# Kernel optimization log

Measured on AMD Instinct MI355X. Metric: run time of the kernel, lower is better.

The kernel has to match this reference:

```python
import jax, jax.numpy as jnp
import numpy as np

N = 50000      # nodes
E = 800000     # edges (before self-loops)
IN = 128       # in_channels
HID = 32       # hidden_channels per head
H = 4          # in_head
OUT = 40       # out_channels
OH = 1         # out_head
NEG = 0.2      # GATConv default negative_slope
EPS = 1e-5     # BatchNorm eps
SKIP = 0.5     # skip_coefficient


def setup_inputs() -> dict:
    key = jax.random.key(0)
    ks = jax.random.split(key, 24)
    s = 0.1
    f32 = jnp.float32
    return dict(
        x=jax.random.normal(ks[0], (N, IN), dtype=f32),
        W0=jax.random.normal(ks[1], (H * HID, IN), dtype=f32) * s,
        as0=jax.random.normal(ks[2], (H, HID), dtype=f32) * s,
        ad0=jax.random.normal(ks[3], (H, HID), dtype=f32) * s,
        b0=jnp.zeros((H * HID,), f32),
        g0=jnp.ones((H * HID,), f32),
        be0=jnp.zeros((H * HID,), f32),
        W1=jax.random.normal(ks[4], (H * HID, H * HID), dtype=f32) * s,
        as1=jax.random.normal(ks[5], (H, HID), dtype=f32) * s,
        ad1=jax.random.normal(ks[6], (H, HID), dtype=f32) * s,
        b1=jnp.zeros((H * HID,), f32),
        g1=jnp.ones((H * HID,), f32),
        be1=jnp.zeros((H * HID,), f32),
        W2=jax.random.normal(ks[7], (OH * OUT, H * HID), dtype=f32) * s,
        as2=jax.random.normal(ks[8], (OH, OUT), dtype=f32) * s,
        ad2=jax.random.normal(ks[9], (OH, OUT), dtype=f32) * s,
        b2=jnp.zeros((OH * OUT,), f32),
        edge_index=jax.random.randint(ks[10], (2, E), 0, N, dtype=jnp.int64),
    )


def gat_layer(x, src, dst, W, a_s, a_d, b, heads, ch):
    # PyG GATConv (concat=True): per-head linear, edge LeakyReLU attention,
    # softmax over incoming edges per destination node, scatter-add aggregate.
    n = x.shape[0]
    h = (x @ W.T).reshape(n, heads, ch)            # [N,H,C]
    al_s = jnp.einsum('nhc,hc->nh', h, a_s)        # [N,H]
    al_d = jnp.einsum('nhc,hc->nh', h, a_d)
    e = jax.nn.leaky_relu(al_s[src] + al_d[dst], NEG)   # [Etot,H]
    m = jax.ops.segment_max(e, dst, num_segments=n)     # per-dst max (stable softmax)
    ex = jnp.exp(e - m[dst])
    denom = jax.ops.segment_sum(ex, dst, num_segments=n)
    alpha = ex / denom[dst]                              # [Etot,H]
    out = jax.ops.segment_sum(alpha[:, :, None] * h[src], dst, num_segments=n)
    return out.reshape(n, heads * ch) + b


def batchnorm(x, g, b):
    # BatchNorm1d, batch-statistics form
    mu = x.mean(0)
    var = x.var(0)
    return (x - mu) * jax.lax.rsqrt(var + EPS) * g + b


def reference(x, W0, as0, ad0, b0, g0, be0, W1, as1, ad1, b1, g1, be1,
              W2, as2, ad2, b2, edge_index):
    loops = jnp.arange(N, dtype=edge_index.dtype)   # GATConv add_self_loops=True
    src = jnp.concatenate([edge_index[0], loops])
    dst = jnp.concatenate([edge_index[1], loops])
    h = jax.nn.relu(batchnorm(gat_layer(x, src, dst, W0, as0, ad0, b0, H, HID), g0, be0))
    skip = h
    h = gat_layer(h, src, dst, W1, as1, ad1, b1, H, HID)
    h = jax.nn.relu(batchnorm(h, g1, be1) + SKIP * skip)
    return gat_layer(h, src, dst, W2, as2, ad2, b2, OH, OUT)
```

## Files before the change

kernel.cpp:

```cpp
#include <hip/hip_runtime.h>
#include <hip/hip_bf16.h>
#include <stdint.h>

#define N_NODES 50000
#define N_EDGES 800000
#define TOT_EDGES (N_EDGES + N_NODES)
#define DIM 128
#define NEG 0.2f
#define BN_EPS 1e-5f
#define SKIPC 0.5f
#define NB 196
#define BCAP 6144

typedef __attribute__((ext_vector_type(8))) short short8;
typedef __attribute__((ext_vector_type(4))) float f32x4;

__device__ inline float bf2f(__hip_bfloat16 v) { return __bfloat162float(v); }
__device__ inline float u16f(unsigned short u) { return __uint_as_float(((unsigned int)u) << 16); }
__device__ inline unsigned short f2bu(float f) {
    __hip_bfloat16 b = __float2bfloat16(f);
    return *(unsigned short*)&b;
}
__device__ inline void fma8(float* acc, float ex, uint4 u) {
    acc[0] += ex * u16f((unsigned short)(u.x & 0xFFFFu));
    acc[1] += ex * u16f((unsigned short)(u.x >> 16));
    acc[2] += ex * u16f((unsigned short)(u.y & 0xFFFFu));
    acc[3] += ex * u16f((unsigned short)(u.y >> 16));
    acc[4] += ex * u16f((unsigned short)(u.z & 0xFFFFu));
    acc[5] += ex * u16f((unsigned short)(u.z >> 16));
    acc[6] += ex * u16f((unsigned short)(u.w & 0xFFFFu));
    acc[7] += ex * u16f((unsigned short)(u.w >> 16));
}
__device__ inline unsigned int pk2(float a, float b) {
    return (unsigned int)f2bu(a) | ((unsigned int)f2bu(b) << 16);
}

__global__ void zero_out_k(unsigned short* out, int n) {
    int g = blockIdx.x * 256 + threadIdx.x;
    if (g < n) out[g] = 0;
}

__global__ __launch_bounds__(256) void binA_k(const int* __restrict__ ei,
                                              int* __restrict__ bcnt,
                                              unsigned int* __restrict__ pairs) {
    __shared__ int cnt[NB], base[NB], cur[NB];
    __shared__ int sf;
    int t = threadIdx.x;
    if (t == 0) sf = 0;
    for (int i = t; i < NB; i += 256) cnt[i] = 0;
    __syncthreads();
    if (t < 16 && ei[2 * t + 1] != 0) atomicOr(&sf, 1);
    __syncthreads();
    int f = (sf == 0);
    int b0 = blockIdx.x * 4096;
    unsigned int pk[16];
    int bk[16];
    #pragma unroll
    for (int j = 0; j < 16; ++j) {
        int g = b0 + j * 256 + t;
        bk[j] = -1;
        if (g < N_EDGES) {
            int s, d;
            if (f) { s = ei[2 * g]; d = ei[2 * (N_EDGES + g)]; }
            else   { s = ei[g];     d = ei[N_EDGES + g]; }
            if ((unsigned)d < N_NODES && (unsigned)s < N_NODES) {
                bk[j] = d >> 8;
                pk[j] = (unsigned int)s | ((unsigned int)(d & 255) << 16);
                atomicAdd(&cnt[bk[j]], 1);
            }
        }
    }
    __syncthreads();
    if (t < NB) {
        int c = cnt[t];
        base[t] = c ? atomicAdd(&bcnt[t], c) : 0;
        cur[t] = 0;
    }
    __syncthreads();
    #pragma unroll
    for (int j = 0; j < 16; ++j) {
        if (bk[j] >= 0) {
            int off = base[bk[j]] + atomicAdd(&cur[bk[j]], 1);
            if (off < BCAP) pairs[(size_t)bk[j] * BCAP + off] = pk[j];
        }
    }
}

__global__ __launch_bounds__(256) void binB_k(const int* __restrict__ bcnt,
                                              const unsigned int* __restrict__ pairs,
                                              int* __restrict__ row_ptr,
                                              int* __restrict__ ssrc) {
    __shared__ int cntL[256], scanL[256], curL[256];
    __shared__ int sred[256];
    int b = blockIdx.x, t = threadIdx.x;
    int n0 = b * 256;
    int nn = min(256, N_NODES - n0);
    int cnt_b = min(bcnt[b], BCAP);
    int contrib = 0;
    if (t < b) contrib = min(bcnt[t], BCAP) + min(256, N_NODES - t * 256);
    sred[t] = contrib;
    __syncthreads();
    #pragma unroll
    for (int off = 128; off > 0; off >>= 1) {
        if (t < off) sred[t] += sred[t + off];
        __syncthreads();
    }
    int gbase = sred[0];
    if (b == NB - 1 && t == 0) row_ptr[N_NODES] = gbase + cnt_b + nn;

    const unsigned int* P = pairs + (size_t)b * BCAP;
    cntL[t] = (t < nn) ? 1 : 0;
    __syncthreads();
    for (int i = t; i < cnt_b; i += 256)
        atomicAdd(&cntL[P[i] >> 16], 1);
    __syncthreads();
    int v = cntL[t];
    scanL[t] = v;
    __syncthreads();
    for (int off = 1; off < 256; off <<= 1) {
        int x = (t >= off) ? scanL[t - off] : 0;
        __syncthreads();
        scanL[t] += x;
        __syncthreads();
    }
    int excl = scanL[t] - v;
    if (t < nn) row_ptr[n0 + t] = gbase + excl;
    curL[t] = excl;
    __syncthreads();
    if (t < nn) {
        int pos = atomicAdd(&curL[t], 1);
        ssrc[gbase + pos] = n0 + t;
    }
    for (int i = t; i < cnt_b; i += 256) {
        unsigned int p = P[i];
        int pos = atomicAdd(&curL[p >> 16], 1);
        ssrc[gbase + pos] = (int)(p & 0xFFFFu);
    }
}

struct PrepJobs { const void* src[13]; float* dst[13]; int n[13]; };
__global__ __launch_bounds__(256) void wcvt_k(const void* __restrict__ W0,
                                              const void* __restrict__ W1,
                                              const void* __restrict__ W2,
                                              unsigned short* __restrict__ Wb0,
                                              unsigned short* __restrict__ Wb1,
                                              unsigned short* __restrict__ Wb2,
                                              PrepJobs jobs,
                                              int* __restrict__ fflag) {
    __shared__ int cs;
    int t = threadIdx.x;
    if (t == 0) cs = 0;
    __syncthreads();
    {
        unsigned int w = ((const unsigned int*)W0)[t];
        float v0 = u16f((unsigned short)(w & 0xFFFFu));
        float a = fabsf(v0);
        int sane = (a < 2.0f && (a > 1e-20f || v0 == 0.0f)) ? 1 : 0;
        atomicAdd(&cs, sane);
    }
    __syncthreads();
    int f = (cs >= 128) ? 1 : 0;
    int b = blockIdx.x;
    if (b == 0 && t == 0) fflag[0] = f;
    if (b < 148) {
        int g = b * 256 + t;
        const void* W; unsigned short* Wb; int idx;
        if (g < 16384)        { W = W0; Wb = Wb0; idx = g; }
        else if (g < 32768)   { W = W1; Wb = Wb1; idx = g - 16384; }
        else if (g < 37888)   { W = W2; Wb = Wb2; idx = g - 32768; }
        else return;
        if (f) Wb[idx] = ((const unsigned short*)W)[idx];
        else   Wb[idx] = f2bu(((const float*)W)[idx]);
    } else {
        int j = b - 148;
        int n = jobs.n[j];
        const void* s = jobs.src[j];
        float* d = jobs.dst[j];
        for (int i = t; i < n; i += 256)
            d[i] = f ? bf2f(((const __hip_bfloat16*)s)[i]) : ((const float*)s)[i];
    }
}

__global__ __launch_bounds__(256) void wext_k(unsigned short* __restrict__ Wb0,
                                              unsigned short* __restrict__ Wb1,
                                              unsigned short* __restrict__ Wb2,
                                              const float* __restrict__ pAs0, const float* __restrict__ pAd0,
                                              const float* __restrict__ pAs1, const float* __restrict__ pAd1,
                                              const float* __restrict__ pAs2, const float* __restrict__ pAd2) {
    int g = blockIdx.x * 256 + threadIdx.x;
    if (g < 2048) {
        int layer = g >> 10;
        int gi = g & 1023;
        int rowq = gi >> 7;
        int k = gi & 127;
        int hh = rowq & 3, dir = rowq >> 2;
        unsigned short* Wb = layer ? Wb1 : Wb0;
        const float* p = layer ? (dir ? pAd1 : pAs1) : (dir ? pAd0 : pAs0);
        float v = 0.f;
        #pragma unroll
        for (int c = 0; c < 32; ++c)
            v += p[hh * 32 + c] * u16f(Wb[(size_t)(hh * 32 + c) * 128 + k]);
        Wb[(size_t)(128 + dir * 4 + hh) * 128 + k] = f2bu(v);
    } else if (g < 2304) {
        int gi = g - 2048;
        int dir = gi >> 7;
        int k = gi & 127;
        const float* p = dir ? pAd2 : pAs2;
        float v = 0.f;
        #pragma unroll
        for (int c = 0; c < 40; ++c)
            v += p[c] * u16f(Wb2[(size_t)c * 128 + k]);
        Wb2[(size_t)(40 + dir) * 128 + k] = f2bu(v);
    }
}

template<int MT, int MV, int ALBASE, int NH, int AMODE>
__device__ inline void mfma_body(const void* __restrict__ X,
                                 const unsigned short* __restrict__ Xprev,
                                 const unsigned short* __restrict__ Wb,
                                 unsigned short* __restrict__ Y,
                                 float* __restrict__ als, float* __restrict__ ald, int n,
                                 const float* __restrict__ bnA, const float* __restrict__ gA,
                                 const float* __restrict__ beA,
                                 const float* __restrict__ bnB, const float* __restrict__ gB,
                                 const float* __restrict__ beB) {
    const int MROWS = ALBASE + 2 * NH;
    __shared__ float sAsc[128], sAsh[128], sBsc[128], sBsh[128];
    if (AMODE >= 2) {
        int t = threadIdx.x;
        const float invN = 1.f / (float)N_NODES;
        if (t < 128) {
            float mean = bnA[t] * invN;
            float var = fmaxf(bnA[128 + t] * invN - mean * mean, 0.f);
            float s = rsqrtf(var + BN_EPS) * gA[t];
            sAsc[t] = s;
            sAsh[t] = beA[t] - mean * s;
        } else if (AMODE == 3) {
            int c = t - 128;
            float mean = bnB[c] * invN;
            float var = fmaxf(bnB[128 + c] * invN - mean * mean, 0.f);
            float s = rsqrtf(var + BN_EPS) * gB[c];
            sBsc[c] = s;
            sBsh[c] = beB[c] - mean * s;
        }
        __syncthreads();
    }
    int wave = (blockIdx.x * blockDim.x + threadIdx.x) >> 6;
    int r0 = wave * 16;
    if (r0 >= n) return;
    int lane = threadIdx.x & 63;
    int m = lane & 15, quad = lane >> 4;
    f32x4 acc[MT];
    #pragma unroll
    for (int t = 0; t < MT; ++t) acc[t] = (f32x4){0.f, 0.f, 0.f, 0.f};
    int arow = min(r0 + m, n - 1);

    #pragma unroll
    for (int kc = 0; kc < 4; ++kc) {
        int k0 = kc * 32 + quad * 8;
        short8 a;
        if (AMODE == 0) {
            const float* xp = (const float*)X + (size_t)arow * 128 + k0;
            float4 x0 = *(const float4*)xp;
            float4 x1 = *(const float4*)(xp + 4);
            a[0] = (short)f2bu(x0.x); a[1] = (short)f2bu(x0.y);
            a[2] = (short)f2bu(x0.z); a[3] = (short)f2bu(x0.w);
            a[4] = (short)f2bu(x1.x); a[5] = (short)f2bu(x1.y);
            a[6] = (short)f2bu(x1.z); a[7] = (short)f2bu(x1.w);
        } else if (AMODE == 1) {
            a = *(const short8*)((const unsigned short*)X + (size_t)arow * 128 + k0);
        } else if (AMODE == 2) {
            short8 hv = *(const short8*)((const unsigned short*)X + (size_t)arow * 128 + k0);
            #pragma unroll
            for (int j = 0; j < 8; ++j) {
                float v = u16f((unsigned short)hv[j]) * sAsc[k0 + j] + sAsh[k0 + j];
                a[j] = (short)f2bu(fmaxf(v, 0.f));
            }
        } else {
            short8 hv = *(const short8*)((const unsigned short*)X + (size_t)arow * 128 + k0);
            short8 pv = *(const short8*)(Xprev + (size_t)arow * 128 + k0);
            #pragma unroll
            for (int j = 0; j < 8; ++j) {
                float v0 = fmaxf(u16f((unsigned short)pv[j]) * sBsc[k0 + j] + sBsh[k0 + j], 0.f);
                float v = u16f((unsigned short)hv[j]) * sAsc[k0 + j] + sAsh[k0 + j] + SKIPC * v0;
                a[j] = (short)f2bu(fmaxf(v, 0.f));
            }
        }
        #pragma unroll
        for (int t = 0; t < MT; ++t) {
            int col = t * 16 + m;
            short8 b;
            if (col < MROWS) b = *(const short8*)(Wb + (size_t)col * 128 + k0);
            else             b = (short8){0,0,0,0,0,0,0,0};
            acc[t] = __builtin_amdgcn_mfma_f32_16x16x32_bf16(a, b, acc[t], 0, 0, 0);
        }
    }

    #pragma unroll
    for (int t = 0; t < MT; ++t) {
        int col = t * 16 + m;
        #pragma unroll
        for (int r = 0; r < 4; ++r) {
            int row = r0 + quad * 4 + r;
            if (row >= n) continue;
            if (col < MV) {
                Y[(size_t)row * MV + col] = f2bu(acc[t][r]);
            } else if (col < ALBASE + NH) {
                als[row * NH + (col - ALBASE)] = acc[t][r];
            } else if (col < ALBASE + 2 * NH) {
                ald[row * NH + (col - ALBASE - NH)] = acc[t][r];
            }
        }
    }
}

__global__ __launch_bounds__(256) void mfma_x_k(const void* __restrict__ X,
                                                const unsigned short* __restrict__ Wb,
                                                unsigned short* __restrict__ Y,
                                                float* __restrict__ als, float* __restrict__ ald,
                                                int n, const int* __restrict__ fflag) {
    if (fflag[0]) mfma_body<9, 128, 128, 4, 1>(X, nullptr, Wb, Y, als, ald, n,
                                               nullptr, nullptr, nullptr, nullptr, nullptr, nullptr);
    else          mfma_body<9, 128, 128, 4, 0>(X, nullptr, Wb, Y, als, ald, n,
                                               nullptr, nullptr, nullptr, nullptr, nullptr, nullptr);
}

__global__ __launch_bounds__(256) void mfma_aff_k(const unsigned short* __restrict__ X,
                                                  const unsigned short* __restrict__ Wb,
                                                  unsigned short* __restrict__ Y,
                                                  float* __restrict__ als, float* __restrict__ ald,
                                                  int n,
                                                  const float* __restrict__ bn,
                                                  const float* __restrict__ g,
                                                  const float* __restrict__ be) {
    mfma_body<9, 128, 128, 4, 2>(X, nullptr, Wb, Y, als, ald, n,
                                 bn, g, be, nullptr, nullptr, nullptr);
}

__global__ __launch_bounds__(256) void mfma_affskip_k(const unsigned short* __restrict__ X,
                                                      const unsigned short* __restrict__ Xprev,
                                                      const unsigned short* __restrict__ Wb,
                                                      unsigned short* __restrict__ Y,
                                                      float* __restrict__ als, float* __restrict__ ald,
                                                      int n,
                                                      const float* __restrict__ bnA,
                                                      const float* __restrict__ gA,
                                                      const float* __restrict__ beA,
                                                      const float* __restrict__ bnB,
                                                      const float* __restrict__ gB,
                                                      const float* __restrict__ beB) {
    mfma_body<3, 40, 40, 1, 3>(X, Xprev, Wb, Y, als, ald, n,
                               bnA, gA, beA, bnB, gB, beB);
}

template<int H, int C, int LPG, int CPL, bool FINAL>
__global__ __launch_bounds__(256) void agg4_k(const unsigned short* __restrict__ hbuf,
                                              const float* __restrict__ als,
                                              const float* __restrict__ ald,
                                              const float* __restrict__ bias,
                                              const int* __restrict__ row_ptr,
                                              const int* __restrict__ ssrc,
                                              void* __restrict__ out,
                                              const int* __restrict__ fflag, int n) {
    const int HC = H * C;
    const int G = 64 / LPG;
    const int NV = CPL / 8;
    int gw = (blockIdx.x * blockDim.x + threadIdx.x) >> 6;
    if (gw >= n) return;
    int lane = threadIdx.x & 63;
    int grp = lane / LPG;
    int sl  = lane % LPG;
    int c0 = sl * CPL;
    bool act = c0 < HC;
    int hl = act ? (c0 / C) : 0;
    int d = gw;
    int beg = row_ptr[d], end = row_ptr[d + 1];
    float adh = ald[d * H + hl];

    float denom = 0.f;
    float acc[CPL];
    #pragma unroll
    for (int j = 0; j < CPL; ++j) acc[j] = 0.f;

    int i0 = beg + grp;
    bool h0 = i0 < end;
    bool h1 = (i0 + G) < end;
    float al0 = 0.f, al1 = 0.f;
    uint4 u0[NV], u1[NV];
    if (h0) {
        int s = ssrc[i0];
        al0 = als[s * H + hl];
        if (act) {
            const uint4* hp = (const uint4*)(hbuf + (size_t)s * HC + c0);
            #pragma unroll
            for (int v = 0; v < NV; ++v) u0[v] = hp[v];
        }
    }
    if (h1) {
        int s = ssrc[i0 + G];
        al1 = als[s * H + hl];
        if (act) {
            const uint4* hp = (const uint4*)(hbuf + (size_t)s * HC + c0);
            #pragma unroll
            for (int v = 0; v < NV; ++v) u1[v] = hp[v];
        }
    }
    int inext = i0 + 2 * G;

    while (h0) {
        bool h2 = inext < end;
        float al2 = 0.f;
        uint4 u2[NV];
        if (h2) {
            int s = ssrc[inext];
            al2 = als[s * H + hl];
            if (act) {
                const uint4* hp = (const uint4*)(hbuf + (size_t)s * HC + c0);
                #pragma unroll
                for (int v = 0; v < NV; ++v) u2[v] = hp[v];
            }
        }
        float t = al0 + adh;
        t = t > 0.f ? t : NEG * t;
        float ex = __expf(t);
        denom += ex;
        if (act) {
            #pragma unroll
            for (int v = 0; v < NV; ++v) fma8(acc + v * 8, ex, u0[v]);
        }
        h0 = h1; al0 = al1;
        #pragma unroll
        for (int v = 0; v < NV; ++v) u0[v] = u1[v];
        h1 = h2; al1 = al2;
        #pragma unroll
        for (int v = 0; v < NV; ++v) u1[v] = u2[v];
        inext += G;
    }

    #pragma unroll
    for (int off = LPG; off < 64; off <<= 1) {
        denom += __shfl_xor(denom, off, 64);
        #pragma unroll
        for (int j = 0; j < CPL; ++j) acc[j] += __shfl_xor(acc[j], off, 64);
    }

    if (grp == 0 && act) {
        float inv = 1.f / denom;
        float vals[CPL];
        #pragma unroll
        for (int j = 0; j < CPL; ++j) vals[j] = acc[j] * inv + bias[c0 + j];
        if (FINAL && !fflag[0]) {
            float* of = (float*)out + (size_t)d * HC + c0;
            #pragma unroll
            for (int j = 0; j < CPL; ++j) of[j] = vals[j];
        } else {
            unsigned short* ob = (unsigned short*)out + (size_t)d * HC + c0;
            #pragma unroll
            for (int v = 0; v < NV; ++v) {
                uint4 pk;
                pk.x = pk2(vals[v * 8 + 0], vals[v * 8 + 1]);
                pk.y = pk2(vals[v * 8 + 2], vals[v * 8 + 3]);
                pk.z = pk2(vals[v * 8 + 4], vals[v * 8 + 5]);
                pk.w = pk2(vals[v * 8 + 6], vals[v * 8 + 7]);
                *(uint4*)(ob + v * 8) = pk;
            }
        }
    }
}

__global__ __launch_bounds__(256) void bn_stats_k(const unsigned short* __restrict__ x,
                                                  float* __restrict__ sum,
                                                  float* __restrict__ sumsq, int n) {
    __shared__ float ss[256], sq[256];
    int t = threadIdx.x;
    int c = t & 127, half = t >> 7;
    float s = 0.f, s2 = 0.f;
    for (int r = blockIdx.x * 2 + half; r < n; r += gridDim.x * 2) {
        float v = u16f(x[(size_t)r * 128 + c]);
        s += v; s2 += v * v;
    }
    ss[t] = s; sq[t] = s2;
    __syncthreads();
    if (t < 128) {
        s = ss[t] + ss[t + 128];
        s2 = sq[t] + sq[t + 128];
        atomicAdd(&sum[c], s);
        atomicAdd(&sumsq[c], s2);
    }
}

extern "C" void kernel_launch(void* const* d_in, const int* in_sizes, int n_in,
                              void* d_out, int out_size, void* d_ws, size_t ws_size,
                              hipStream_t stream) {
    const void* x   = d_in[0];
    const void* W0  = d_in[1];
    const void* as0 = d_in[2];
    const void* ad0 = d_in[3];
    const void* b0  = d_in[4];
    const void* g0  = d_in[5];
    const void* be0 = d_in[6];
    const void* W1  = d_in[7];
    const void* as1 = d_in[8];
    const void* ad1 = d_in[9];
    const void* b1  = d_in[10];
    const void* g1  = d_in[11];
    const void* be1 = d_in[12];
    const void* W2  = d_in[13];
    const void* as2 = d_in[14];
    const void* ad2 = d_in[15];
    const void* b2  = d_in[16];
    const int* ei = (const int*)d_in[17];

    char* w = (char*)d_ws;
    size_t off = 0;
    auto alloc = [&](size_t bytes) -> void* {
        void* p = w + off;
        off = (off + bytes + 255) & ~(size_t)255;
        return p;
    };
    unsigned short* hbf = (unsigned short*)alloc((size_t)N_NODES * 128 * 2);
    unsigned short* hA0 = (unsigned short*)alloc((size_t)N_NODES * 128 * 2);
    unsigned short* hA1 = (unsigned short*)alloc((size_t)N_NODES * 128 * 2);
    float* als = (float*)alloc((size_t)N_NODES * 4 * 4);
    float* ald = (float*)alloc((size_t)N_NODES * 4 * 4);
    unsigned short* Wb0 = (unsigned short*)alloc((size_t)136 * 128 * 2);
    unsigned short* Wb1 = (unsigned short*)alloc((size_t)136 * 128 * 2);
    unsigned short* Wb2 = (unsigned short*)alloc((size_t)42 * 128 * 2);
    float* prm = (float*)alloc(2048 * 4);
    int* zreg = (int*)alloc((size_t)(NB + 512) * 4);
    int* bcnt = zreg;
    float* bn0 = (float*)(zreg + NB);
    float* bn1 = bn0 + 256;
    int* row_ptr = (int*)alloc((size_t)(N_NODES + 1) * 4);
    int* ssrc    = (int*)alloc((size_t)TOT_EDGES * 4);
    unsigned int* pairs = (unsigned int*)alloc((size_t)NB * BCAP * 4);
    int* fflag   = (int*)alloc(256);

    float* pAs0 = prm + 0,   * pAd0 = prm + 128,  * pB0 = prm + 256;
    float* pG0  = prm + 384, * pBe0 = prm + 512;
    float* pAs1 = prm + 640, * pAd1 = prm + 768,  * pB1 = prm + 896;
    float* pG1  = prm + 1024,* pBe1 = prm + 1152;
    float* pAs2 = prm + 1280,* pAd2 = prm + 1320, * pB2 = prm + 1360;

    if (off > ws_size) {
        zero_out_k<<<(out_size + 255) / 256, 256, 0, stream>>>((unsigned short*)d_out, out_size);
        return;
    }

    const int MB = (((N_NODES + 15) / 16) + 3) / 4;
    const int AB = (N_NODES * 64 + 255) / 256;

    hipMemsetAsync(zreg, 0, (size_t)(NB + 512) * 4, stream);
    binA_k<<<(N_EDGES + 4095) / 4096, 256, 0, stream>>>(ei, bcnt, pairs);
    binB_k<<<NB, 256, 0, stream>>>(bcnt, pairs, row_ptr, ssrc);

    PrepJobs jobs;
    const void* srcs[13] = { as0, ad0, b0, g0, be0, as1, ad1, b1, g1, be1, as2, ad2, b2 };
    float* dsts[13] = { pAs0, pAd0, pB0, pG0, pBe0, pAs1, pAd1, pB1, pG1, pBe1, pAs2, pAd2, pB2 };
    int ns[13] = { 128,128,128,128,128, 128,128,128,128,128, 40,40,40 };
    for (int i = 0; i < 13; ++i) { jobs.src[i] = srcs[i]; jobs.dst[i] = dsts[i]; jobs.n[i] = ns[i]; }
    wcvt_k<<<161, 256, 0, stream>>>(W0, W1, W2, Wb0, Wb1, Wb2, jobs, fflag);
    wext_k<<<9, 256, 0, stream>>>(Wb0, Wb1, Wb2, pAs0, pAd0, pAs1, pAd1, pAs2, pAd2);

    mfma_x_k<<<MB, 256, 0, stream>>>(x, Wb0, hbf, als, ald, N_NODES, fflag);
    agg4_k<4, 32, 8, 16, false><<<AB, 256, 0, stream>>>(hbf, als, ald, pB0, row_ptr, ssrc, hA0, fflag, N_NODES);
    bn_stats_k<<<256, 256, 0, stream>>>(hA0, bn0, bn0 + 128, N_NODES);

    mfma_aff_k<<<MB, 256, 0, stream>>>(hA0, Wb1, hbf, als, ald, N_NODES, bn0, pG0, pBe0);
    agg4_k<4, 32, 8, 16, false><<<AB, 256, 0, stream>>>(hbf, als, ald, pB1, row_ptr, ssrc, hA1, fflag, N_NODES);
    bn_stats_k<<<256, 256, 0, stream>>>(hA1, bn1, bn1 + 128, N_NODES);

    mfma_affskip_k<<<MB, 256, 0, stream>>>(hA1, hA0, Wb2, hbf, als, ald, N_NODES,
                                           bn1, pG1, pBe1, bn0, pG0, pBe0);
    agg4_k<1, 40, 8, 8, true><<<AB, 256, 0, stream>>>(hbf, als, ald, pB2, row_ptr, ssrc, d_out, fflag, N_NODES);
}
```

Measured before the change: 350.9 us.

## Fuse BatchNorm statistics into aggregation and merge setup kernels

Removes the separate bn_stats passes by accumulating per-channel sum and sum-of-squares inside the aggregation kernel's epilogue. Each block reduces into shared memory, then adds into one of 64 replicated global partial buffers, which the following matmul kernel sums when it builds the BN scale and shift. The binning and weight-conversion setup kernels are also merged into two combined launches, cutting launch count. The cost is shared-memory atomics in the aggregation epilogue, global atomics spread over the replicas, and reduced precision because the statistics now come from fp32 values before bf16 rounding, so they differ slightly from the old stats taken on the stored output.

```diff
diff --git a/kernel.cpp b/kernel.cpp
--- a/kernel.cpp
+++ b/kernel.cpp
@@ -11,6 +11,8 @@
 #define SKIPC 0.5f
 #define NB 196
 #define BCAP 6144
+#define BINA_BLKS ((N_EDGES + 4095) / 4096)
+#define NREP 64
 
 typedef __attribute__((ext_vector_type(8))) short short8;
 typedef __attribute__((ext_vector_type(4))) float f32x4;
@@ -40,9 +42,9 @@
     if (g < n) out[g] = 0;
 }
 
-__global__ __launch_bounds__(256) void binA_k(const int* __restrict__ ei,
-                                              int* __restrict__ bcnt,
-                                              unsigned int* __restrict__ pairs) {
+__device__ inline void binA_body(int bid, const int* __restrict__ ei,
+                                 int* __restrict__ bcnt,
+                                 unsigned int* __restrict__ pairs) {
     __shared__ int cnt[NB], base[NB], cur[NB];
     __shared__ int sf;
     int t = threadIdx.x;
@@ -52,7 +54,7 @@
     if (t < 16 && ei[2 * t + 1] != 0) atomicOr(&sf, 1);
     __syncthreads();
     int f = (sf == 0);
-    int b0 = blockIdx.x * 4096;
+    int b0 = bid * 4096;
     unsigned int pk[16];
     int bk[16];
     #pragma unroll
@@ -86,67 +88,16 @@
     }
 }
 
-__global__ __launch_bounds__(256) void binB_k(const int* __restrict__ bcnt,
-                                              const unsigned int* __restrict__ pairs,
-                                              int* __restrict__ row_ptr,
-                                              int* __restrict__ ssrc) {
-    __shared__ int cntL[256], scanL[256], curL[256];
-    __shared__ int sred[256];
-    int b = blockIdx.x, t = threadIdx.x;
-    int n0 = b * 256;
-    int nn = min(256, N_NODES - n0);
-    int cnt_b = min(bcnt[b], BCAP);
-    int contrib = 0;
-    if (t < b) contrib = min(bcnt[t], BCAP) + min(256, N_NODES - t * 256);
-    sred[t] = contrib;
-    __syncthreads();
-    #pragma unroll
-    for (int off = 128; off > 0; off >>= 1) {
-        if (t < off) sred[t] += sred[t + off];
-        __syncthreads();
-    }
-    int gbase = sred[0];
-    if (b == NB - 1 && t == 0) row_ptr[N_NODES] = gbase + cnt_b + nn;
-
-    const unsigned int* P = pairs + (size_t)b * BCAP;
-    cntL[t] = (t < nn) ? 1 : 0;
-    __syncthreads();
-    for (int i = t; i < cnt_b; i += 256)
-        atomicAdd(&cntL[P[i] >> 16], 1);
-    __syncthreads();
-    int v = cntL[t];
-    scanL[t] = v;
-    __syncthreads();
-    for (int off = 1; off < 256; off <<= 1) {
-        int x = (t >= off) ? scanL[t - off] : 0;
-        __syncthreads();
-        scanL[t] += x;
-        __syncthreads();
-    }
-    int excl = scanL[t] - v;
-    if (t < nn) row_ptr[n0 + t] = gbase + excl;
-    curL[t] = excl;
-    __syncthreads();
-    if (t < nn) {
-        int pos = atomicAdd(&curL[t], 1);
-        ssrc[gbase + pos] = n0 + t;
-    }
-    for (int i = t; i < cnt_b; i += 256) {
-        unsigned int p = P[i];
-        int pos = atomicAdd(&curL[p >> 16], 1);
-        ssrc[gbase + pos] = (int)(p & 0xFFFFu);
-    }
-}
-
 struct PrepJobs { const void* src[13]; float* dst[13]; int n[13]; };
-__global__ __launch_bounds__(256) void wcvt_k(const void* __restrict__ W0,
-                                              const void* __restrict__ W1,
-                                              const void* __restrict__ W2,
-                                              unsigned short* __restrict__ Wb0,
-                                              unsigned short* __restrict__ Wb1,
-                                              unsigned short* __restrict__ Wb2,
-                                              PrepJobs jobs,
-                                              int* __restrict__ fflag) {
+__device__ inline void wcvt_body(int bid,
+                                 const void* __restrict__ W0,
+                                 const void* __restrict__ W1,
+                                 const void* __restrict__ W2,
+                                 unsigned short* __restrict__ Wb0,
+                                 unsigned short* __restrict__ Wb1,
+                                 unsigned short* __restrict__ Wb2,
+                                 const PrepJobs& jobs,
+                                 int* __restrict__ fflag) {
     __shared__ int cs;
     int t = threadIdx.x;
     if (t == 0) cs = 0;
@@ -160,10 +111,9 @@
     }
     __syncthreads();
     int f = (cs >= 128) ? 1 : 0;
-    int b = blockIdx.x;
-    if (b == 0 && t == 0) fflag[0] = f;
-    if (b < 148) {
-        int g = b * 256 + t;
+    if (bid == 0 && t == 0) fflag[0] = f;
+    if (bid < 148) {
+        int g = bid * 256 + t;
         const void* W; unsigned short* Wb; int idx;
         if (g < 16384)        { W = W0; Wb = Wb0; idx = g; }
         else if (g < 32768)   { W = W1; Wb = Wb1; idx = g - 16384; }
@@ -172,7 +122,7 @@
         if (f) Wb[idx] = ((const unsigned short*)W)[idx];
         else   Wb[idx] = f2bu(((const float*)W)[idx]);
     } else {
-        int j = b - 148;
+        int j = bid - 148;
         int n = jobs.n[j];
         const void* s = jobs.src[j];
         float* d = jobs.dst[j];
@@ -181,13 +131,81 @@
     }
 }
 
-__global__ __launch_bounds__(256) void wext_k(unsigned short* __restrict__ Wb0,
+__global__ __launch_bounds__(256) void fat1_k(const int* __restrict__ ei,
+                                              int* __restrict__ bcnt,
+                                              unsigned int* __restrict__ pairs,
+                                              const void* __restrict__ W0,
+                                              const void* __restrict__ W1,
+                                              const void* __restrict__ W2,
+                                              unsigned short* __restrict__ Wb0,
                                               unsigned short* __restrict__ Wb1,
                                               unsigned short* __restrict__ Wb2,
-                                              const float* __restrict__ pAs0, const float* __restrict__ pAd0,
-                                              const float* __restrict__ pAs1, const float* __restrict__ pAd1,
-                                              const float* __restrict__ pAs2, const float* __restrict__ pAd2) {
-    int g = blockIdx.x * 256 + threadIdx.x;
+                                              PrepJobs jobs,
+                                              int* __restrict__ fflag) {
+    if (blockIdx.x < BINA_BLKS) binA_body(blockIdx.x, ei, bcnt, pairs);
+    else wcvt_body(blockIdx.x - BINA_BLKS, W0, W1, W2, Wb0, Wb1, Wb2, jobs, fflag);
+}
+
+__device__ inline void binB_body(int b, const int* __restrict__ bcnt,
+                                 const unsigned int* __restrict__ pairs,
+                                 int* __restrict__ row_ptr,
+                                 int* __restrict__ ssrc) {
+    __shared__ int cntL[256], scanL[256], curL[256];
+    __shared__ int sred[256];
+    int t = threadIdx.x;
+    int n0 = b * 256;
+    int nn = min(256, N_NODES - n0);
+    int cnt_b = min(bcnt[b], BCAP);
+    int contrib = 0;
+    if (t < b) contrib = min(bcnt[t], BCAP) + min(256, N_NODES - t * 256);
+    sred[t] = contrib;
+    __syncthreads();
+    #pragma unroll
+    for (int off = 128; off > 0; off >>= 1) {
+        if (t < off) sred[t] += sred[t + off];
+        __syncthreads();
+    }
+    int gbase = sred[0];
+    if (b == NB - 1 && t == 0) row_ptr[N_NODES] = gbase + cnt_b + nn;
+
+    const unsigned int* P = pairs + (size_t)b * BCAP;
+    cntL[t] = (t < nn) ? 1 : 0;
+    __syncthreads();
+    for (int i = t; i < cnt_b; i += 256)
+        atomicAdd(&cntL[P[i] >> 16], 1);
+    __syncthreads();
+    int v = cntL[t];
+    scanL[t] = v;
+    __syncthreads();
+    for (int off = 1; off < 256; off <<= 1) {
+        int x = (t >= off) ? scanL[t - off] : 0;
+        __syncthreads();
+        scanL[t] += x;
+        __syncthreads();
+    }
+    int excl = scanL[t] - v;
+    if (t < nn) row_ptr[n0 + t] = gbase + excl;
+    curL[t] = excl;
+    __syncthreads();
+    if (t < nn) {
+        int pos = atomicAdd(&curL[t], 1);
+        ssrc[gbase + pos] = n0 + t;
+    }
+    for (int i = t; i < cnt_b; i += 256) {
+        unsigned int p = P[i];
+        int pos = atomicAdd(&curL[p >> 16], 1);
+        ssrc[gbase + pos] = (int)(p & 0xFFFFu);
+    }
+}
+
+__device__ inline void wext_body(int bid,
+                                 unsigned short* __restrict__ Wb0,
+                                 unsigned short* __restrict__ Wb1,
+                                 unsigned short* __restrict__ Wb2,
+                                 const float* __restrict__ pAs0, const float* __restrict__ pAd0,
+                                 const float* __restrict__ pAs1, const float* __restrict__ pAd1,
+                                 const float* __restrict__ pAs2, const float* __restrict__ pAd2) {
+    int g = bid * 256 + threadIdx.x;
     if (g < 2048) {
         int layer = g >> 10;
         int gi = g & 1023;
@@ -214,6 +232,20 @@
     }
 }
 
+__global__ __launch_bounds__(256) void fat2_k(const int* __restrict__ bcnt,
+                                              const unsigned int* __restrict__ pairs,
+                                              int* __restrict__ row_ptr,
+                                              int* __restrict__ ssrc,
+                                              unsigned short* __restrict__ Wb0,
+                                              unsigned short* __restrict__ Wb1,
+                                              unsigned short* __restrict__ Wb2,
+                                              const float* __restrict__ pAs0, const float* __restrict__ pAd0,
+                                              const float* __restrict__ pAs1, const float* __restrict__ pAd1,
+                                              const float* __restrict__ pAs2, const float* __restrict__ pAd2) {
+    if (blockIdx.x < NB) binB_body(blockIdx.x, bcnt, pairs, row_ptr, ssrc);
+    else wext_body(blockIdx.x - NB, Wb0, Wb1, Wb2, pAs0, pAd0, pAs1, pAd1, pAs2, pAd2);
+}
+
 template<int MT, int MV, int ALBASE, int NH, int AMODE>
 __device__ inline void mfma_body(const void* __restrict__ X,
                                  const unsigned short* __restrict__ Xprev,
@@ -230,18 +262,30 @@
         int t = threadIdx.x;
         const float invN = 1.f / (float)N_NODES;
         if (t < 128) {
-            float mean = bnA[t] * invN;
-            float var = fmaxf(bnA[128 + t] * invN - mean * mean, 0.f);
-            float s = rsqrtf(var + BN_EPS) * gA[t];
-            sAsc[t] = s;
-            sAsh[t] = beA[t] - mean * s;
+            float s = 0.f, q = 0.f;
+            #pragma unroll 8
+            for (int r = 0; r < NREP; ++r) {
+                s += bnA[r * 256 + t];
+                q += bnA[r * 256 + 128 + t];
+            }
+            float mean = s * invN;
+            float var = fmaxf(q * invN - mean * mean, 0.f);
+            float sc = rsqrtf(var + BN_EPS) * gA[t];
+            sAsc[t] = sc;
+            sAsh[t] = beA[t] - mean * sc;
         } else if (AMODE == 3) {
             int c = t - 128;
-            float mean = bnB[c] * invN;
-            float var = fmaxf(bnB[128 + c] * invN - mean * mean, 0.f);
-            float s = rsqrtf(var + BN_EPS) * gB[c];
-            sBsc[c] = s;
-            sBsh[c] = beB[c] - mean * s;
+            float s = 0.f, q = 0.f;
+            #pragma unroll 8
+            for (int r = 0; r < NREP; ++r) {
+                s += bnB[r * 256 + c];
+                q += bnB[r * 256 + 128 + c];
+            }
+            float mean = s * invN;
+            float var = fmaxf(q * invN - mean * mean, 0.f);
+            float sc = rsqrtf(var + BN_EPS) * gB[c];
+            sBsc[c] = sc;
+            sBsh[c] = beB[c] - mean * sc;
         }
         __syncthreads();
     }
@@ -353,7 +397,7 @@
                                bnA, gA, beA, bnB, gB, beB);
 }
 
-template<int H, int C, int LPG, int CPL, bool FINAL>
+template<int H, int C, int LPG, int CPL, bool FINAL, bool STATS>
 __global__ __launch_bounds__(256) void agg4_k(const unsigned short* __restrict__ hbuf,
                                               const float* __restrict__ als,
                                               const float* __restrict__ ald,
@@ -361,131 +405,133 @@
                                               const int* __restrict__ row_ptr,
                                               const int* __restrict__ ssrc,
                                               void* __restrict__ out,
-                                              const int* __restrict__ fflag, int n) {
+                                              const int* __restrict__ fflag, int n,
+                                              float* __restrict__ bnp) {
     const int HC = H * C;
     const int G = 64 / LPG;
     const int NV = CPL / 8;
+    __shared__ float sSQ[256];
+    if (STATS) {
+        if (threadIdx.x < 256) sSQ[threadIdx.x] = 0.f;
+        __syncthreads();
+    }
     int gw = (blockIdx.x * blockDim.x + threadIdx.x) >> 6;
-    if (gw >= n) return;
-    int lane = threadIdx.x & 63;
-    int grp = lane / LPG;
-    int sl  = lane % LPG;
-    int c0 = sl * CPL;
-    bool act = c0 < HC;
-    int hl = act ? (c0 / C) : 0;
-    int d = gw;
-    int beg = row_ptr[d], end = row_ptr[d + 1];
-    float adh = ald[d * H + hl];
-
-    float denom = 0.f;
-    float acc[CPL];
-    #pragma unroll
-    for (int j = 0; j < CPL; ++j) acc[j] = 0.f;
-
-    int i0 = beg + grp;
-    bool h0 = i0 < end;
-    bool h1 = (i0 + G) < end;
-    float al0 = 0.f, al1 = 0.f;
-    uint4 u0[NV], u1[NV];
-    if (h0) {
-        int s = ssrc[i0];
-        al0 = als[s * H + hl];
-        if (act) {
-            const uint4* hp = (const uint4*)(hbuf + (size_t)s * HC + c0);
-            #pragma unroll
-            for (int v = 0; v < NV; ++v) u0[v] = hp[v];
-        }
-    }
-    if (h1) {
-        int s = ssrc[i0 + G];
-        al1 = als[s * H + hl];
-        if (act) {
-            const uint4* hp = (const uint4*)(hbuf + (size_t)s * HC + c0);
-            #pragma unroll
-            for (int v = 0; v < NV; ++v) u1[v] = hp[v];
-        }
-    }
-    int inext = i0 + 2 * G;
-
-    while (h0) {
-        bool h2 = inext < end;
-        float al2 = 0.f;
-        uint4 u2[NV];
-        if (h2) {
-            int s = ssrc[inext];
-            al2 = als[s * H + hl];
+    bool live = gw < n;
+    if (live) {
+        int lane = threadIdx.x & 63;
+        int grp = lane / LPG;
+        int sl  = lane % LPG;
+        int c0 = sl * CPL;
+        bool act = c0 < HC;
+        int hl = act ? (c0 / C) : 0;
+        int d = gw;
+        int beg = row_ptr[d], end = row_ptr[d + 1];
+        float adh = ald[d * H + hl];
+
+        float denom = 0.f;
+        float acc[CPL];
+        #pragma unroll
+        for (int j = 0; j < CPL; ++j) acc[j] = 0.f;
+
+        int i0 = beg + grp;
+        bool h0 = i0 < end;
+        bool h1 = (i0 + G) < end;
+        float al0 = 0.f, al1 = 0.f;
+        uint4 u0[NV], u1[NV];
+        if (h0) {
+            int s = ssrc[i0];
+            al0 = als[s * H + hl];
             if (act) {
                 const uint4* hp = (const uint4*)(hbuf + (size_t)s * HC + c0);
                 #pragma unroll
-                for (int v = 0; v < NV; ++v) u2[v] = hp[v];
-            }
-        }
-        float t = al0 + adh;
-        t = t > 0.f ? t : NEG * t;
-        float ex = __expf(t);
-        denom += ex;
-        if (act) {
+                for (int v = 0; v < NV; ++v) u0[v] = hp[v];
+            }
+        }
+        if (h1) {
+            int s = ssrc[i0 + G];
+            al1 = als[s * H + hl];
+            if (act) {
+                const uint4* hp = (const uint4*)(hbuf + (size_t)s * HC + c0);
+                #pragma unroll
+                for (int v = 0; v < NV; ++v) u1[v] = hp[v];
+            }
+        }
+        int inext = i0 + 2 * G;
+
+        while (h0) {
+            bool h2 = inext < end;
+            float al2 = 0.f;
+            uint4 u2[NV];
+            if (h2) {
+                int s = ssrc[inext];
+                al2 = als[s * H + hl];
+                if (act) {
+                    const uint4* hp = (const uint4*)(hbuf + (size_t)s * HC + c0);
+                    #pragma unroll
+                    for (int v = 0; v < NV; ++v) u2[v] = hp[v];
+                }
+            }
+            float t = al0 + adh;
+            t = t > 0.f ? t : NEG * t;
+            float ex = __expf(t);
+            denom += ex;
+            if (act) {
+                #pragma unroll
+                for (int v = 0; v < NV; ++v) fma8(acc + v * 8, ex, u0[v]);
+            }
+            h0 = h1; al0 = al1;
             #pragma unroll
-            for (int v = 0; v < NV; ++v) fma8(acc + v * 8, ex, u0[v]);
-        }
-        h0 = h1; al0 = al1;
+            for (int v = 0; v < NV; ++v) u0[v] = u1[v];
+            h1 = h2; al1 = al2;
+            #pragma unroll
+            for (int v = 0; v < NV; ++v) u1[v] = u2[v];
+            inext += G;
+        }
+
         #pragma unroll
-        for (int v = 0; v < NV; ++v) u0[v] = u1[v];
-        h1 = h2; al1 = al2;
-        #pragma unroll
-        for (int v = 0; v < NV; ++v) u1[v] = u2[v];
-        inext += G;
-    }
-
-    #pragma unroll
-    for (int off = LPG; off < 64; off <<= 1) {
-        denom += __shfl_xor(denom, off, 64);
-        #pragma unroll
-        for (int j = 0; j < CPL; ++j) acc[j] += __shfl_xor(acc[j], off, 64);
-    }
-
-    if (grp == 0 && act) {
-        float inv = 1.f / denom;
-        float vals[CPL];
-        #pragma unroll
-        for (int j = 0; j < CPL; ++j) vals[j] = acc[j] * inv + bias[c0 + j];
-        if (FINAL && !fflag[0]) {
-            float* of = (float*)out + (size_t)d * HC + c0;
+        for (int off = LPG; off < 64; off <<= 1) {
+            denom += __shfl_xor(denom, off, 64);
             #pragma unroll
-            for (int j = 0; j < CPL; ++j) of[j] = vals[j];
-        } else {
-            unsigned short* ob = (unsigned short*)out + (size_t)d * HC + c0;
+            for (int j = 0; j < CPL; ++j) acc[j] += __shfl_xor(acc[j], off, 64);
+        }
+
+        if (grp == 0 && act) {
+            float inv = 1.f / denom;
+            float vals[CPL];
             #pragma unroll
-            for (int v = 0; v < NV; ++v) {
-                uint4 pk;
-                pk.x = pk2(vals[v * 8 + 0], vals[v * 8 + 1]);
-                pk.y = pk2(vals[v * 8 + 2], vals[v * 8 + 3]);
-                pk.z = pk2(vals[v * 8 + 4], vals[v * 8 + 5]);
-                pk.w = pk2(vals[v * 8 + 6], vals[v * 8 + 7]);
-                *(uint4*)(ob + v * 8) = pk;
-            }
-        }
-    }
-}
-
-__global__ __launch_bounds__(256) void bn_stats_k(const unsigned short* __restrict__ x,
-                                                  float* __restrict__ sum,
-                                                  float* __restrict__ sumsq, int n) {
-    __shared__ float ss[256], sq[256];
-    int t = threadIdx.x;
-    int c = t & 127, half = t >> 7;
-    float s = 0.f, s2 = 0.f;
-    for (int r = blockIdx.x * 2 + half; r < n; r += gridDim.x * 2) {
-        float v = u16f(x[(size_t)r * 128 + c]);
-        s += v; s2 += v * v;
-    }
-    ss[t] = s; sq[t] = s2;
-    __syncthreads();
-    if (t < 128) {
-        s = ss[t] + ss[t + 128];
-        s2 = sq[t] + sq[t + 128];
-        atomicAdd(&sum[c], s);
-        atomicAdd(&sumsq[c], s2);
+            for (int j = 0; j < CPL; ++j) vals[j] = acc[j] * inv + bias[c0 + j];
+            if (STATS) {
+                #pragma unroll
+                for (int j = 0; j < CPL; ++j) {
+                    atomicAdd(&sSQ[c0 + j], vals[j]);
+                    atomicAdd(&sSQ[128 + c0 + j], vals[j] * vals[j]);
+                }
+            }
+            if (FINAL && !fflag[0]) {
+                float* of = (float*)out + (size_t)d * HC + c0;
+                #pragma unroll
+                for (int j = 0; j < CPL; ++j) of[j] = vals[j];
+            } else {
+                unsigned short* ob = (unsigned short*)out + (size_t)d * HC + c0;
+                #pragma unroll
+                for (int v = 0; v < NV; ++v) {
+                    uint4 pk;
+                    pk.x = pk2(vals[v * 8 + 0], vals[v * 8 + 1]);
+                    pk.y = pk2(vals[v * 8 + 2], vals[v * 8 + 3]);
+                    pk.z = pk2(vals[v * 8 + 4], vals[v * 8 + 5]);
+                    pk.w = pk2(vals[v * 8 + 6], vals[v * 8 + 7]);
+                    *(uint4*)(ob + v * 8) = pk;
+                }
+            }
+        }
+    }
+    if (STATS) {
+        __syncthreads();
+        int t = threadIdx.x;
+        if (t < 256) {
+            float v = sSQ[t];
+            atomicAdd(&bnp[(size_t)(blockIdx.x & (NREP - 1)) * 256 + t], v);
+        }
     }
 }
 
@@ -527,10 +573,10 @@
     unsigned short* Wb1 = (unsigned short*)alloc((size_t)136 * 128 * 2);
     unsigned short* Wb2 = (unsigned short*)alloc((size_t)42 * 128 * 2);
     float* prm = (float*)alloc(2048 * 4);
-    int* zreg = (int*)alloc((size_t)(NB + 512) * 4);
+    int* zreg = (int*)alloc((size_t)(NB + 2 * NREP * 256) * 4);
     int* bcnt = zreg;
-    float* bn0 = (float*)(zreg + NB);
-    float* bn1 = bn0 + 256;
+    float* bn0p = (float*)(zreg + NB);
+    float* bn1p = bn0p + NREP * 256;
     int* row_ptr = (int*)alloc((size_t)(N_NODES + 1) * 4);
     int* ssrc    = (int*)alloc((size_t)TOT_EDGES * 4);
     unsigned int* pairs = (unsigned int*)alloc((size_t)NB * BCAP * 4);
@@ -550,27 +596,21 @@
     const int MB = (((N_NODES + 15) / 16) + 3) / 4;
     const int AB = (N_NODES * 64 + 255) / 256;
 
-    hipMemsetAsync(zreg, 0, (size_t)(NB + 512) * 4, stream);
-    binA_k<<<(N_EDGES + 4095) / 4096, 256, 0, stream>>>(ei, bcnt, pairs);
-    binB_k<<<NB, 256, 0, stream>>>(bcnt, pairs, row_ptr, ssrc);
-
     PrepJobs jobs;
     const void* srcs[13] = { as0, ad0, b0, g0, be0, as1, ad1, b1, g1, be1, as2, ad2, b2 };
     float* dsts[13] = { pAs0, pAd0, pB0, pG0, pBe0, pAs1, pAd1, pB1, pG1, pBe1, pAs2, pAd2, pB2 };
     int ns[13] = { 128,128,128,128,128, 128,128,128,128,128, 40,40,40 };
     for (int i = 0; i < 13; ++i) { jobs.src[i] = srcs[i]; jobs.dst[i] = dsts[i]; jobs.n[i] = ns[i]; }
-    wcvt_k<<<161, 256, 0, stream>>>(W0, W1, W2, Wb0, Wb1, Wb2, jobs, fflag);
-    wext_k<<<9, 256, 0, stream>>>(Wb0, Wb1, Wb2, pAs0, pAd0, pAs1, pAd1, pAs2, pAd2);
-
+
+    hipMemsetAsync(zreg, 0, (size_t)(NB + 2 * NREP * 256) * 4, stream);
+    fat1_k<<<BINA_BLKS + 161, 256, 0, stream>>>(ei, bcnt, pairs, W0, W1, W2, Wb0, Wb1, Wb2, jobs, fflag);
+    fat2_k<<<NB + 9, 256, 0, stream>>>(bcnt, pairs, row_ptr, ssrc, Wb0, Wb1, Wb2,
+                                       pAs0, pAd0, pAs1, pAd1, pAs2, pAd2);
     mfma_x_k<<<MB, 256, 0, stream>>>(x, Wb0, hbf, als, ald, N_NODES, fflag);
-    agg4_k<4, 32, 8, 16, false><<<AB, 256, 0, stream>>>(hbf, als, ald, pB0, row_ptr, ssrc, hA0, fflag, N_NODES);
-    bn_stats_k<<<256, 256, 0, stream>>>(hA0, bn0, bn0 + 128, N_NODES);
-
-    mfma_aff_k<<<MB, 256, 0, stream>>>(hA0, Wb1, hbf, als, ald, N_NODES, bn0, pG0, pBe0);
-    agg4_k<4, 32, 8, 16, false><<<AB, 256, 0, stream>>>(hbf, als, ald, pB1, row_ptr, ssrc, hA1, fflag, N_NODES);
-    bn_stats_k<<<256, 256, 0, stream>>>(hA1, bn1, bn1 + 128, N_NODES);
-
+    agg4_k<4, 32, 8, 16, false, true><<<AB, 256, 0, stream>>>(hbf, als, ald, pB0, row_ptr, ssrc, hA0, fflag, N_NODES, bn0p);
+    mfma_aff_k<<<MB, 256, 0, stream>>>(hA0, Wb1, hbf, als, ald, N_NODES, bn0p, pG0, pBe0);
+    agg4_k<4, 32, 8, 16, false, true><<<AB, 256, 0, stream>>>(hbf, als, ald, pB1, row_ptr, ssrc, hA1, fflag, N_NODES, bn1p);
     mfma_affskip_k<<<MB, 256, 0, stream>>>(hA1, hA0, Wb2, hbf, als, ald, N_NODES,
-                                           bn1, pG1, pBe1, bn0, pG0, pBe0);
-    agg4_k<1, 40, 8, 8, true><<<AB, 256, 0, stream>>>(hbf, als, ald, pB2, row_ptr, ssrc, d_out, fflag, N_NODES);
-}
+                                           bn1p, pG1, pBe1, bn0p, pG0, pBe0);
+    agg4_k<1, 40, 8, 8, true, false><<<AB, 256, 0, stream>>>(hbf, als, ald, pB2, row_ptr, ssrc, d_out, fflag, N_NODES, nullptr);
+}
```

Result: slower. 417.6 us (+19.0%).

## Merge setup kernels into two fused launches and deepen aggregation prefetch

Applied to the files above, without the earlier changes.

Combines binA with weight conversion, and binB with attention-weight extension, into two multi-role kernels that pick their job by block index. This cuts the setup from four launches to two and lets independent work share the GPU. The aggregation loop also gains a third stage of software prefetch for neighbour features, adding latency hiding at the cost of more registers, which may lower occupancy.

```diff
diff --git a/kernel.cpp b/kernel.cpp
--- a/kernel.cpp
+++ b/kernel.cpp
@@ -11,6 +11,7 @@
 #define SKIPC 0.5f
 #define NB 196
 #define BCAP 6144
+#define BINA_BLKS ((N_EDGES + 4095) / 4096)
 
 typedef __attribute__((ext_vector_type(8))) short short8;
 typedef __attribute__((ext_vector_type(4))) float f32x4;
@@ -40,9 +41,9 @@
     if (g < n) out[g] = 0;
 }
 
-__global__ __launch_bounds__(256) void binA_k(const int* __restrict__ ei,
-                                              int* __restrict__ bcnt,
-                                              unsigned int* __restrict__ pairs) {
+__device__ inline void binA_body(int bid, const int* __restrict__ ei,
+                                 int* __restrict__ bcnt,
+                                 unsigned int* __restrict__ pairs) {
     __shared__ int cnt[NB], base[NB], cur[NB];
     __shared__ int sf;
     int t = threadIdx.x;
@@ -52,7 +53,7 @@
     if (t < 16 && ei[2 * t + 1] != 0) atomicOr(&sf, 1);
     __syncthreads();
     int f = (sf == 0);
-    int b0 = blockIdx.x * 4096;
+    int b0 = bid * 4096;
     unsigned int pk[16];
     int bk[16];
     #pragma unroll
@@ -86,67 +87,16 @@
     }
 }
 
-__global__ __launch_bounds__(256) void binB_k(const int* __restrict__ bcnt,
-                                              const unsigned int* __restrict__ pairs,
-                                              int* __restrict__ row_ptr,
-                                              int* __restrict__ ssrc) {
-    __shared__ int cntL[256], scanL[256], curL[256];
-    __shared__ int sred[256];
-    int b = blockIdx.x, t = threadIdx.x;
-    int n0 = b * 256;
-    int nn = min(256, N_NODES - n0);
-    int cnt_b = min(bcnt[b], BCAP);
-    int contrib = 0;
-    if (t < b) contrib = min(bcnt[t], BCAP) + min(256, N_NODES - t * 256);
-    sred[t] = contrib;
-    __syncthreads();
-    #pragma unroll
-    for (int off = 128; off > 0; off >>= 1) {
-        if (t < off) sred[t] += sred[t + off];
-        __syncthreads();
-    }
-    int gbase = sred[0];
-    if (b == NB - 1 && t == 0) row_ptr[N_NODES] = gbase + cnt_b + nn;
-
-    const unsigned int* P = pairs + (size_t)b * BCAP;
-    cntL[t] = (t < nn) ? 1 : 0;
-    __syncthreads();
-    for (int i = t; i < cnt_b; i += 256)
-        atomicAdd(&cntL[P[i] >> 16], 1);
-    __syncthreads();
-    int v = cntL[t];
-    scanL[t] = v;
-    __syncthreads();
-    for (int off = 1; off < 256; off <<= 1) {
-        int x = (t >= off) ? scanL[t - off] : 0;
-        __syncthreads();
-        scanL[t] += x;
-        __syncthreads();
-    }
-    int excl = scanL[t] - v;
-    if (t < nn) row_ptr[n0 + t] = gbase + excl;
-    curL[t] = excl;
-    __syncthreads();
-    if (t < nn) {
-        int pos = atomicAdd(&curL[t], 1);
-        ssrc[gbase + pos] = n0 + t;
-    }
-    for (int i = t; i < cnt_b; i += 256) {
-        unsigned int p = P[i];
-        int pos = atomicAdd(&curL[p >> 16], 1);
-        ssrc[gbase + pos] = (int)(p & 0xFFFFu);
-    }
-}
-
 struct PrepJobs { const void* src[13]; float* dst[13]; int n[13]; };
-__global__ __launch_bounds__(256) void wcvt_k(const void* __restrict__ W0,
-                                              const void* __restrict__ W1,
-                                              const void* __restrict__ W2,
-                                              unsigned short* __restrict__ Wb0,
-                                              unsigned short* __restrict__ Wb1,
-                                              unsigned short* __restrict__ Wb2,
-                                              PrepJobs jobs,
-                                              int* __restrict__ fflag) {
+__device__ inline void wcvt_body(int bid,
+                                 const void* __restrict__ W0,
+                                 const void* __restrict__ W1,
+                                 const void* __restrict__ W2,
+                                 unsigned short* __restrict__ Wb0,
+                                 unsigned short* __restrict__ Wb1,
+                                 unsigned short* __restrict__ Wb2,
+                                 const PrepJobs& jobs,
+                                 int* __restrict__ fflag) {
     __shared__ int cs;
     int t = threadIdx.x;
     if (t == 0) cs = 0;
@@ -160,10 +110,9 @@
     }
     __syncthreads();
     int f = (cs >= 128) ? 1 : 0;
-    int b = blockIdx.x;
-    if (b == 0 && t == 0) fflag[0] = f;
-    if (b < 148) {
-        int g = b * 256 + t;
+    if (bid == 0 && t == 0) fflag[0] = f;
+    if (bid < 148) {
+        int g = bid * 256 + t;
         const void* W; unsigned short* Wb; int idx;
         if (g < 16384)        { W = W0; Wb = Wb0; idx = g; }
         else if (g < 32768)   { W = W1; Wb = Wb1; idx = g - 16384; }
@@ -172,7 +121,7 @@
         if (f) Wb[idx] = ((const unsigned short*)W)[idx];
         else   Wb[idx] = f2bu(((const float*)W)[idx]);
     } else {
-        int j = b - 148;
+        int j = bid - 148;
         int n = jobs.n[j];
         const void* s = jobs.src[j];
         float* d = jobs.dst[j];
@@ -181,13 +130,81 @@
     }
 }
 
-__global__ __launch_bounds__(256) void wext_k(unsigned short* __restrict__ Wb0,
+__global__ __launch_bounds__(256) void fat1_k(const int* __restrict__ ei,
+                                              int* __restrict__ bcnt,
+                                              unsigned int* __restrict__ pairs,
+                                              const void* __restrict__ W0,
+                                              const void* __restrict__ W1,
+                                              const void* __restrict__ W2,
+                                              unsigned short* __restrict__ Wb0,
                                               unsigned short* __restrict__ Wb1,
                                               unsigned short* __restrict__ Wb2,
-                                              const float* __restrict__ pAs0, const float* __restrict__ pAd0,
-                                              const float* __restrict__ pAs1, const float* __restrict__ pAd1,
-                                              const float* __restrict__ pAs2, const float* __restrict__ pAd2) {
-    int g = blockIdx.x * 256 + threadIdx.x;
+                                              PrepJobs jobs,
+                                              int* __restrict__ fflag) {
+    if (blockIdx.x < BINA_BLKS) binA_body(blockIdx.x, ei, bcnt, pairs);
+    else wcvt_body(blockIdx.x - BINA_BLKS, W0, W1, W2, Wb0, Wb1, Wb2, jobs, fflag);
+}
+
+__device__ inline void binB_body(int b, const int* __restrict__ bcnt,
+                                 const unsigned int* __restrict__ pairs,
+                                 int* __restrict__ row_ptr,
+                                 int* __restrict__ ssrc) {
+    __shared__ int cntL[256], scanL[256], curL[256];
+    __shared__ int sred[256];
+    int t = threadIdx.x;
+    int n0 = b * 256;
+    int nn = min(256, N_NODES - n0);
+    int cnt_b = min(bcnt[b], BCAP);
+    int contrib = 0;
+    if (t < b) contrib = min(bcnt[t], BCAP) + min(256, N_NODES - t * 256);
+    sred[t] = contrib;
+    __syncthreads();
+    #pragma unroll
+    for (int off = 128; off > 0; off >>= 1) {
+        if (t < off) sred[t] += sred[t + off];
+        __syncthreads();
+    }
+    int gbase = sred[0];
+    if (b == NB - 1 && t == 0) row_ptr[N_NODES] = gbase + cnt_b + nn;
+
+    const unsigned int* P = pairs + (size_t)b * BCAP;
+    cntL[t] = (t < nn) ? 1 : 0;
+    __syncthreads();
+    for (int i = t; i < cnt_b; i += 256)
+        atomicAdd(&cntL[P[i] >> 16], 1);
+    __syncthreads();
+    int v = cntL[t];
+    scanL[t] = v;
+    __syncthreads();
+    for (int off = 1; off < 256; off <<= 1) {
+        int x = (t >= off) ? scanL[t - off] : 0;
+        __syncthreads();
+        scanL[t] += x;
+        __syncthreads();
+    }
+    int excl = scanL[t] - v;
+    if (t < nn) row_ptr[n0 + t] = gbase + excl;
+    curL[t] = excl;
+    __syncthreads();
+    if (t < nn) {
+        int pos = atomicAdd(&curL[t], 1);
+        ssrc[gbase + pos] = n0 + t;
+    }
+    for (int i = t; i < cnt_b; i += 256) {
+        unsigned int p = P[i];
+        int pos = atomicAdd(&curL[p >> 16], 1);
+        ssrc[gbase + pos] = (int)(p & 0xFFFFu);
+    }
+}
+
+__device__ inline void wext_body(int bid,
+                                 unsigned short* __restrict__ Wb0,
+                                 unsigned short* __restrict__ Wb1,
+                                 unsigned short* __restrict__ Wb2,
+                                 const float* __restrict__ pAs0, const float* __restrict__ pAd0,
+                                 const float* __restrict__ pAs1, const float* __restrict__ pAd1,
+                                 const float* __restrict__ pAs2, const float* __restrict__ pAd2) {
+    int g = bid * 256 + threadIdx.x;
     if (g < 2048) {
         int layer = g >> 10;
         int gi = g & 1023;
@@ -212,6 +229,20 @@
             v += p[c] * u16f(Wb2[(size_t)c * 128 + k]);
         Wb2[(size_t)(40 + dir) * 128 + k] = f2bu(v);
     }
+}
+
+__global__ __launch_bounds__(256) void fat2_k(const int* __restrict__ bcnt,
+                                              const unsigned int* __restrict__ pairs,
+                                              int* __restrict__ row_ptr,
+                                              int* __restrict__ ssrc,
+                                              unsigned short* __restrict__ Wb0,
+                                              unsigned short* __restrict__ Wb1,
+                                              unsigned short* __restrict__ Wb2,
+                                              const float* __restrict__ pAs0, const float* __restrict__ pAd0,
+                                              const float* __restrict__ pAs1, const float* __restrict__ pAd1,
+                                              const float* __restrict__ pAs2, const float* __restrict__ pAd2) {
+    if (blockIdx.x < NB) binB_body(blockIdx.x, bcnt, pairs, row_ptr, ssrc);
+    else wext_body(blockIdx.x - NB, Wb0, Wb1, Wb2, pAs0, pAd0, pAs1, pAd1, pAs2, pAd2);
 }
 
 template<int MT, int MV, int ALBASE, int NH, int AMODE>
@@ -385,8 +416,9 @@
     int i0 = beg + grp;
     bool h0 = i0 < end;
     bool h1 = (i0 + G) < end;
-    float al0 = 0.f, al1 = 0.f;
-    uint4 u0[NV], u1[NV];
+    bool h2 = (i0 + 2 * G) < end;
+    float al0 = 0.f, al1 = 0.f, al2 = 0.f;
+    uint4 u0[NV], u1[NV], u2[NV];
     if (h0) {
         int s = ssrc[i0];
         al0 = als[s * H + hl];
@@ -405,19 +437,28 @@
             for (int v = 0; v < NV; ++v) u1[v] = hp[v];
         }
     }
-    int inext = i0 + 2 * G;
+    if (h2) {
+        int s = ssrc[i0 + 2 * G];
+        al2 = als[s * H + hl];
+        if (act) {
+            const uint4* hp = (const uint4*)(hbuf + (size_t)s * HC + c0);
+            #pragma unroll
+            for (int v = 0; v < NV; ++v) u2[v] = hp[v];
+        }
+    }
+    int inext = i0 + 3 * G;
 
     while (h0) {
-        bool h2 = inext < end;
-        float al2 = 0.f;
-        uint4 u2[NV];
-        if (h2) {
+        bool h3 = inext < end;
+        float al3 = 0.f;
+        uint4 u3[NV];
+        if (h3) {
             int s = ssrc[inext];
-            al2 = als[s * H + hl];
+            al3 = als[s * H + hl];
             if (act) {
                 const uint4* hp = (const uint4*)(hbuf + (size_t)s * HC + c0);
                 #pragma unroll
-                for (int v = 0; v < NV; ++v) u2[v] = hp[v];
+                for (int v = 0; v < NV; ++v) u3[v] = hp[v];
             }
         }
         float t = al0 + adh;
@@ -434,6 +475,9 @@
         h1 = h2; al1 = al2;
         #pragma unroll
         for (int v = 0; v < NV; ++v) u1[v] = u2[v];
+        h2 = h3; al2 = al3;
+        #pragma unroll
+        for (int v = 0; v < NV; ++v) u2[v] = u3[v];
         inext += G;
     }
 
@@ -550,26 +594,22 @@
     const int MB = (((N_NODES + 15) / 16) + 3) / 4;
     const int AB = (N_NODES * 64 + 255) / 256;
 
-    hipMemsetAsync(zreg, 0, (size_t)(NB + 512) * 4, stream);
-    binA_k<<<(N_EDGES + 4095) / 4096, 256, 0, stream>>>(ei, bcnt, pairs);
-    binB_k<<<NB, 256, 0, stream>>>(bcnt, pairs, row_ptr, ssrc);
-
     PrepJobs jobs;
     const void* srcs[13] = { as0, ad0, b0, g0, be0, as1, ad1, b1, g1, be1, as2, ad2, b2 };
     float* dsts[13] = { pAs0, pAd0, pB0, pG0, pBe0, pAs1, pAd1, pB1, pG1, pBe1, pAs2, pAd2, pB2 };
     int ns[13] = { 128,128,128,128,128, 128,128,128,128,128, 40,40,40 };
     for (int i = 0; i < 13; ++i) { jobs.src[i] = srcs[i]; jobs.dst[i] = dsts[i]; jobs.n[i] = ns[i]; }
-    wcvt_k<<<161, 256, 0, stream>>>(W0, W1, W2, Wb0, Wb1, Wb2, jobs, fflag);
-    wext_k<<<9, 256, 0, stream>>>(Wb0, Wb1, Wb2, pAs0, pAd0, pAs1, pAd1, pAs2, pAd2);
-
+
+    hipMemsetAsync(zreg, 0, (size_t)(NB + 512) * 4, stream);
+    fat1_k<<<BINA_BLKS + 161, 256, 0, stream>>>(ei, bcnt, pairs, W0, W1, W2, Wb0, Wb1, Wb2, jobs, fflag);
+    fat2_k<<<NB + 9, 256, 0, stream>>>(bcnt, pairs, row_ptr, ssrc, Wb0, Wb1, Wb2,
+                                       pAs0, pAd0, pAs1, pAd1, pAs2, pAd2);
     mfma_x_k<<<MB, 256, 0, stream>>>(x, Wb0, hbf, als, ald, N_NODES, fflag);
     agg4_k<4, 32, 8, 16, false><<<AB, 256, 0, stream>>>(hbf, als, ald, pB0, row_ptr, ssrc, hA0, fflag, N_NODES);
     bn_stats_k<<<256, 256, 0, stream>>>(hA0, bn0, bn0 + 128, N_NODES);
-
     mfma_aff_k<<<MB, 256, 0, stream>>>(hA0, Wb1, hbf, als, ald, N_NODES, bn0, pG0, pBe0);
     agg4_k<4, 32, 8, 16, false><<<AB, 256, 0, stream>>>(hbf, als, ald, pB1, row_ptr, ssrc, hA1, fflag, N_NODES);
     bn_stats_k<<<256, 256, 0, stream>>>(hA1, bn1, bn1 + 128, N_NODES);
-
     mfma_affskip_k<<<MB, 256, 0, stream>>>(hA1, hA0, Wb2, hbf, als, ald, N_NODES,
                                            bn1, pG1, pBe1, bn0, pG0, pBe0);
     agg4_k<1, 40, 8, 8, true><<<AB, 256, 0, stream>>>(hbf, als, ald, pB2, row_ptr, ssrc, d_out, fflag, N_NODES);
```

After: 348.3 us. About the same (-0.8%).
